# Kernel tuning notes

Hardware: AMD Instinct MI355X
Metric: run time of the kernel (lower is better)

Reference implementation:

```python
import jax, jax.numpy as jnp
import numpy as np

N_NODES = 50_000
N_EDGES = 1_600_000
N_VMS = 10_000
N_SCORE = 1_000_000
D_IN, D_E, D_OUT = 128, 64, 64
MLP_IN, MLP_H, MLP_OUT = 64, 128, 64
H1, H2 = 50, 25  # GNNTower fixed hidden widths


def setup_inputs() -> dict:
    key = jax.random.key(0)
    ks = jax.random.split(key, 24)
    w = lambda k, s: (jax.random.normal(k, s, jnp.float32) * 0.05)
    return {
        "component_features": jax.random.normal(ks[0], (N_NODES, D_IN), jnp.float32),
        "component_edges_features": jax.random.normal(ks[1], (N_EDGES, D_E), jnp.float32),
        "vm_features": jax.random.normal(ks[2], (N_VMS, MLP_IN), jnp.float32),
        "src": jax.random.randint(ks[3], (N_EDGES,), 0, N_NODES, jnp.int32),
        "dst": jax.random.randint(ks[4], (N_EDGES,), 0, N_NODES, jnp.int32),
        "e_comp": jax.random.randint(ks[5], (N_SCORE,), 0, N_NODES, jnp.int32),
        "e_vm": jax.random.randint(ks[6], (N_SCORE,), 0, N_VMS, jnp.int32),
        # GNN layer 1: W_msg [D_IN+D_E, H1], W_apply [D_IN+H1, H1]
        "Wm1": w(ks[7], (D_IN + D_E, H1)), "bm1": jnp.zeros((H1,), jnp.float32),
        "Wa1": w(ks[8], (D_IN + H1, H1)), "ba1": jnp.zeros((H1,), jnp.float32),
        # GNN layer 2
        "Wm2": w(ks[9], (H1 + D_E, H2)), "bm2": jnp.zeros((H2,), jnp.float32),
        "Wa2": w(ks[10], (H1 + H2, H2)), "ba2": jnp.zeros((H2,), jnp.float32),
        # GNN layer 3
        "Wm3": w(ks[11], (H2 + D_E, D_OUT)), "bm3": jnp.zeros((D_OUT,), jnp.float32),
        "Wa3": w(ks[12], (H2 + D_OUT, D_OUT)), "ba3": jnp.zeros((D_OUT,), jnp.float32),
        # MLP tower
        "Wmlp1": w(ks[13], (MLP_IN, MLP_H)), "bmlp1": jnp.zeros((MLP_H,), jnp.float32),
        "Wmlp2": w(ks[14], (MLP_H, MLP_OUT)), "bmlp2": jnp.zeros((MLP_OUT,), jnp.float32),
    }


def reference(component_features, component_edges_features, vm_features,
              src, dst, e_comp, e_vm,
              Wm1, bm1, Wa1, ba1, Wm2, bm2, Wa2, ba2, Wm3, bm3, Wa3, ba3,
              Wmlp1, bmlp1, Wmlp2, bmlp2):
    ef = component_edges_features

    def gnn_layer(h, Wm, bm, Wa, ba):
        d = h.shape[-1]
        # message: relu(W_msg @ concat(h[src], efeat)) == gather + split matmul (avoids concat copy)
        m = jax.nn.relu(h[src] @ Wm[:d] + ef @ Wm[d:] + bm)  # [E, out]
        # scatter-sum aggregation into destination nodes
        h_neigh = jax.ops.segment_sum(m, dst, num_segments=N_NODES)  # [N, out]
        # apply: relu(W_apply @ concat(h, h_neigh))
        return jax.nn.relu(h @ Wa[:d] + h_neigh @ Wa[d:] + ba)

    h = gnn_layer(component_features, Wm1, bm1, Wa1, ba1)   # [N, 50]
    h = gnn_layer(h, Wm2, bm2, Wa2, ba2)                    # [N, 25]  (dropout = identity in eval)
    h = gnn_layer(h, Wm3, bm3, Wa3, ba3)                    # [N, D_OUT]

    vm = jax.nn.relu(vm_features @ Wmlp1 + bmlp1) @ Wmlp2 + bmlp2  # [V, MLP_OUT]

    # sum over concat(comp_emb[e_comp], vm_emb[e_vm]) == sum of parts
    scores = jnp.sum(h, axis=-1)[e_comp] + jnp.sum(vm, axis=-1)[e_vm]  # [N_SCORE]
    return jax.nn.sigmoid(scores)
```

## Files before the change

### kernel.cpp

```cpp
#include <hip/hip_runtime.h>

typedef unsigned int uint;
typedef unsigned short ushort;
typedef short bf16x8 __attribute__((ext_vector_type(8)));
typedef float f32x4  __attribute__((ext_vector_type(4)));


__device__ __forceinline__ ushort f2bf(float f) {
    uint u = __float_as_uint(f);
    u += 0x7FFFu + ((u >> 16) & 1u);
    return (ushort)(u >> 16);
}
__device__ __forceinline__ float bf2f(uint s) {
    return __uint_as_float(s << 16);
}

template<int K0, int KP0, int K1, int KP1, int KC, int OUT, int WOUT,
         int NTC, int RPT, int MODE>
__global__ __launch_bounds__(256) void tile_gemm(
    const float* __restrict__ X0, int sx0,
    const float* __restrict__ X1, int sx1,
    const float* __restrict__ Wg, const float* __restrict__ Bg,
    float* __restrict__ Y, int sy, int nR)
{
    constexpr int KPT  = KP0 + KP1;
    constexpr int C4   = KC / 4;
    constexpr int OUTP = 4 * NTC;
    constexpr int NTR  = 256 / NTC;
    constexpr int TR   = NTR * RPT;
    static_assert(TR == 128, "tile must be 128 rows");
    static_assert(KPT % KC == 0, "KC must divide KPT");

    __shared__ float4 Xl[TR * C4];
    __shared__ float4 Wl[KC * NTC];
    __shared__ float  __align__(16) bl[OUTP];

    const int tid = threadIdx.x;
    const int r0  = blockIdx.x * TR;

    for (int idx = tid; idx < OUTP; idx += 256)
        bl[idx] = (Bg != nullptr && idx < OUT) ? Bg[idx] : 0.f;

    const int tc  = tid & (NTC - 1);
    const int tr  = tid / NTC;
    const int key = (RPT * tr) >> 3;

    float4 acc[RPT];
    #pragma unroll
    for (int i = 0; i < RPT; i++) acc[i] = make_float4(0.f, 0.f, 0.f, 0.f);

    for (int kc0 = 0; kc0 < KPT; kc0 += KC) {
        if (kc0 != 0) __syncthreads();
        for (int idx = tid; idx < TR * C4; idx += 256) {
            int r = idx / C4, c = idx - r * C4;
            int col = kc0 + 4 * c;
            int gr = r0 + r;
            float4 v = make_float4(0.f, 0.f, 0.f, 0.f);
            if (gr < nR) {
                if (KP1 == 0 || col < KP0)
                    v = *reinterpret_cast<const float4*>(X0 + (long long)gr * sx0 + col);
                else
                    v = *reinterpret_cast<const float4*>(X1 + (long long)gr * sx1 + (col - KP0));
            }
            int cs = c + ((r >> 3) % C4); if (cs >= C4) cs -= C4;
            Xl[r * C4 + cs] = v;
        }
        for (int idx = tid; idx < KC * OUTP; idx += 256) {
            int kl = idx / OUTP, o = idx - kl * OUTP;
            int k = kc0 + kl;
            float v = 0.f;
            if (o < OUT) {
                if (k < KP0) { if (k < K0) v = Wg[k * OUT + o]; }
                else { int kk = k - KP0; if (kk < K1) v = Wg[(K0 + kk) * OUT + o]; }
            }
            ((float*)Wl)[kl * OUTP + o] = v;
        }
        __syncthreads();

        const int km = key % C4;
        #pragma unroll 4
        for (int k4 = 0; k4 < C4; k4++) {
            int cs = k4 + km; if (cs >= C4) cs -= C4;
            float4 x[RPT];
            #pragma unroll
            for (int i = 0; i < RPT; i++)
                x[i] = Xl[(RPT * tr + i) * C4 + cs];
            #pragma unroll
            for (int kk = 0; kk < 4; kk++) {
                float4 w = Wl[(4 * k4 + kk) * NTC + tc];
                #pragma unroll
                for (int i = 0; i < RPT; i++) {
                    float xs = (kk == 0) ? x[i].x : (kk == 1) ? x[i].y
                             : (kk == 2) ? x[i].z : x[i].w;
                    acc[i].x = fmaf(xs, w.x, acc[i].x);
                    acc[i].y = fmaf(xs, w.y, acc[i].y);
                    acc[i].z = fmaf(xs, w.z, acc[i].z);
                    acc[i].w = fmaf(xs, w.w, acc[i].w);
                }
            }
        }
    }

    const float4 b4 = reinterpret_cast<float4*>(bl)[tc];
    const int o = 4 * tc;

    if (MODE == 0 || MODE == 1) {
        if (o < WOUT) {
            #pragma unroll
            for (int i = 0; i < RPT; i++) {
                int gr = r0 + RPT * tr + i;
                if (gr < nR) {
                    float4 v;
                    v.x = acc[i].x + b4.x; v.y = acc[i].y + b4.y;
                    v.z = acc[i].z + b4.z; v.w = acc[i].w + b4.w;
                    if (MODE == 1) {
                        v.x = fmaxf(v.x, 0.f); v.y = fmaxf(v.y, 0.f);
                        v.z = fmaxf(v.z, 0.f); v.w = fmaxf(v.w, 0.f);
                    }
                    *reinterpret_cast<float4*>(Y + (long long)gr * sy + o) = v;
                }
            }
        }
    } else {
        #pragma unroll
        for (int i = 0; i < RPT; i++) {
            int gr = r0 + RPT * tr + i;
            float s = fmaxf(acc[i].x + b4.x, 0.f) + fmaxf(acc[i].y + b4.y, 0.f)
                    + fmaxf(acc[i].z + b4.z, 0.f) + fmaxf(acc[i].w + b4.w, 0.f);
            #pragma unroll
            for (int off = 1; off < NTC; off <<= 1) s += __shfl_xor(s, off);
            if (tc == 0 && gr < nR) Y[gr] = s;
        }
    }
}

template<int NT, bool SECB>
__global__ __launch_bounds__(256) void proj_mfma(
    const float* __restrict__ ef,
    const float* __restrict__ WA, int wacols,
    const float* __restrict__ WB, int wbcols,
    const int* __restrict__ invperm,
    ushort* __restrict__ GA, ushort* __restrict__ GB, int nE)
{
    constexpr int NCOL = NT * 16;
    constexpr int CLP  = NCOL + 8;
    constexpr int CPR  = NCOL / 8;
    constexpr int GAS  = SECB ? 64 : NCOL;

    __shared__ ushort Al[64 * 64];
    __shared__ ushort Bl[NT * 128 * 8];
    __shared__ ushort Cl[64 * CLP];
    __shared__ int    sl_pos[64];

    const int tid = threadIdx.x;

    for (int idx = tid; idx < NT * 128; idx += 256) {
        int t  = idx >> 7;
        int ks = (idx >> 6) & 1;
        int l  = idx & 63;
        int col = t * 16 + (l & 15);
        int kb  = ks * 32 + ((l >> 4) << 3);
        ushort u[8];
        #pragma unroll
        for (int j = 0; j < 8; j++) {
            int k = kb + j;
            float w = 0.f;
            if (!SECB || col < 64) { if (col < wacols) w = WA[k * wacols + col]; }
            else { int c2 = col - 64; if (c2 < wbcols) w = WB[k * wbcols + c2]; }
            u[j] = f2bf(w);
        }
        *reinterpret_cast<bf16x8*>(&Bl[idx * 8]) = *reinterpret_cast<bf16x8*>(u);
    }

    const int wv = tid >> 6;
    const int l  = tid & 63;
    const int ntiles = (nE + 63) >> 6;

    for (int tile = blockIdx.x; tile < ntiles; tile += gridDim.x) {
        const int r0 = tile << 6;
        __syncthreads();

        if (tid < 64) sl_pos[tid] = (r0 + tid < nE) ? invperm[r0 + tid] : -1;
        {
            int row = tid >> 2;
            int kq  = (tid & 3) << 4;
            int gr  = r0 + row;
            float4 f0 = {0,0,0,0}, f1 = {0,0,0,0}, f2 = {0,0,0,0}, f3 = {0,0,0,0};
            if (gr < nE) {
                const float* p = ef + (size_t)gr * 64 + kq;
                f0 = *reinterpret_cast<const float4*>(p);
                f1 = *reinterpret_cast<const float4*>(p + 4);
                f2 = *reinterpret_cast<const float4*>(p + 8);
                f3 = *reinterpret_cast<const float4*>(p + 12);
            }
            ushort u[16];
            u[0]=f2bf(f0.x); u[1]=f2bf(f0.y); u[2]=f2bf(f0.z); u[3]=f2bf(f0.w);
            u[4]=f2bf(f1.x); u[5]=f2bf(f1.y); u[6]=f2bf(f1.z); u[7]=f2bf(f1.w);
            u[8]=f2bf(f2.x); u[9]=f2bf(f2.y); u[10]=f2bf(f2.z); u[11]=f2bf(f2.w);
            u[12]=f2bf(f3.x); u[13]=f2bf(f3.y); u[14]=f2bf(f3.z); u[15]=f2bf(f3.w);
            int kc0 = ((kq >> 3) + 0) ^ (row & 7);
            int kc1 = ((kq >> 3) + 1) ^ (row & 7);
            *reinterpret_cast<bf16x8*>(&Al[(row << 6) + kc0 * 8]) = *reinterpret_cast<bf16x8*>(u);
            *reinterpret_cast<bf16x8*>(&Al[(row << 6) + kc1 * 8]) = *reinterpret_cast<bf16x8*>(u + 8);
        }
        __syncthreads();

        f32x4 acc[NT];
        #pragma unroll
        for (int t = 0; t < NT; t++) acc[t] = (f32x4){0.f, 0.f, 0.f, 0.f};
        const int rl = wv * 16 + (l & 15);
        #pragma unroll
        for (int ks = 0; ks < 2; ks++) {
            int kch = (ks * 4 + (l >> 4)) ^ (rl & 7);
            bf16x8 a = *reinterpret_cast<const bf16x8*>(&Al[(rl << 6) + kch * 8]);
            #pragma unroll
            for (int t = 0; t < NT; t++) {
                bf16x8 b = *reinterpret_cast<const bf16x8*>(&Bl[((t * 2 + ks) * 64 + l) * 8]);
                acc[t] = __builtin_amdgcn_mfma_f32_16x16x32_bf16(a, b, acc[t], 0, 0, 0);
            }
        }
        #pragma unroll
        for (int t = 0; t < NT; t++)
            #pragma unroll
            for (int j = 0; j < 4; j++) {
                int rr = wv * 16 + ((l >> 4) << 2) + j;
                Cl[rr * CLP + t * 16 + (l & 15)] = f2bf(acc[t][j]);
            }
        __syncthreads();

        for (int idx = tid; idx < 64 * CPR; idx += 256) {
            int row = idx / CPR, c = idx - row * CPR;
            int pos = sl_pos[row];
            if (pos < 0) continue;
            uint4 v = *reinterpret_cast<const uint4*>(&Cl[row * CLP + c * 8]);
            if (!SECB || c < 8)
                *reinterpret_cast<uint4*>(GA + (size_t)pos * GAS + c * 8) = v;
            else
                *reinterpret_cast<uint4*>(GB + (size_t)pos * 32 + (c - 8) * 8) = v;
        }
    }
}

template<int NCL, int GS, int SP>
__global__ __launch_bounds__(256) void agg_csr(
    const ushort* __restrict__ G, const int* __restrict__ srcp,
    const int* __restrict__ rowp, const float* __restrict__ P,
    float* __restrict__ ng, int nN)
{
    const int o = threadIdx.x & (NCL - 1);
    const int g = threadIdx.x / NCL;
    const int n = blockIdx.x * (256 / NCL) + g;
    if (n >= nN) return;
    const int s0 = rowp[n], s1 = rowp[n + 1];

    float a0=0,a1=0,a2=0,a3=0,a4=0,a5=0,a6=0,a7=0;
    int pos = s0;
    for (; pos + 2 <= s1; pos += 2) {
        int sA = srcp[pos], sB = srcp[pos + 1];
        uint4 gA = *reinterpret_cast<const uint4*>(G + (size_t)pos * GS + o * 8);
        uint4 gB = *reinterpret_cast<const uint4*>(G + (size_t)(pos + 1) * GS + o * 8);
        const float* pA = P + (size_t)sA * SP + o * 8;
        const float* pB = P + (size_t)sB * SP + o * 8;
        float4 pa0 = *reinterpret_cast<const float4*>(pA);
        float4 pa1 = *reinterpret_cast<const float4*>(pA + 4);
        float4 pb0 = *reinterpret_cast<const float4*>(pB);
        float4 pb1 = *reinterpret_cast<const float4*>(pB + 4);
        a0 += fmaxf(pa0.x + bf2f(gA.x & 0xffffu), 0.f) + fmaxf(pb0.x + bf2f(gB.x & 0xffffu), 0.f);
        a1 += fmaxf(pa0.y + bf2f(gA.x >> 16), 0.f)     + fmaxf(pb0.y + bf2f(gB.x >> 16), 0.f);
        a2 += fmaxf(pa0.z + bf2f(gA.y & 0xffffu), 0.f) + fmaxf(pb0.z + bf2f(gB.y & 0xffffu), 0.f);
        a3 += fmaxf(pa0.w + bf2f(gA.y >> 16), 0.f)     + fmaxf(pb0.w + bf2f(gB.y >> 16), 0.f);
        a4 += fmaxf(pa1.x + bf2f(gA.z & 0xffffu), 0.f) + fmaxf(pb1.x + bf2f(gB.z & 0xffffu), 0.f);
        a5 += fmaxf(pa1.y + bf2f(gA.z >> 16), 0.f)     + fmaxf(pb1.y + bf2f(gB.z >> 16), 0.f);
        a6 += fmaxf(pa1.z + bf2f(gA.w & 0xffffu), 0.f) + fmaxf(pb1.z + bf2f(gB.w & 0xffffu), 0.f);
        a7 += fmaxf(pa1.w + bf2f(gA.w >> 16), 0.f)     + fmaxf(pb1.w + bf2f(gB.w >> 16), 0.f);
    }
    if (pos < s1) {
        int sA = srcp[pos];
        uint4 gA = *reinterpret_cast<const uint4*>(G + (size_t)pos * GS + o * 8);
        const float* pA = P + (size_t)sA * SP + o * 8;
        float4 pa0 = *reinterpret_cast<const float4*>(pA);
        float4 pa1 = *reinterpret_cast<const float4*>(pA + 4);
        a0 += fmaxf(pa0.x + bf2f(gA.x & 0xffffu), 0.f);
        a1 += fmaxf(pa0.y + bf2f(gA.x >> 16), 0.f);
        a2 += fmaxf(pa0.z + bf2f(gA.y & 0xffffu), 0.f);
        a3 += fmaxf(pa0.w + bf2f(gA.y >> 16), 0.f);
        a4 += fmaxf(pa1.x + bf2f(gA.z & 0xffffu), 0.f);
        a5 += fmaxf(pa1.y + bf2f(gA.z >> 16), 0.f);
        a6 += fmaxf(pa1.z + bf2f(gA.w & 0xffffu), 0.f);
        a7 += fmaxf(pa1.w + bf2f(gA.w >> 16), 0.f);
    }
    float4 w0 = {a0, a1, a2, a3}, w1 = {a4, a5, a6, a7};
    float* yp = ng + (size_t)n * 64 + o * 8;
    *reinterpret_cast<float4*>(yp)     = w0;
    *reinterpret_cast<float4*>(yp + 4) = w1;
}

__global__ __launch_bounds__(256) void hist_kernel(
    const int* __restrict__ dst, int* __restrict__ deg, int nE)
{
    for (int e = blockIdx.x * 256 + threadIdx.x; e < nE; e += gridDim.x * 256)
        atomicAdd(&deg[dst[e]], 1);
}

__global__ __launch_bounds__(1024) void scan_kernel(
    const int* __restrict__ deg, int* __restrict__ rowp, int nN)
{
    __shared__ int wsum[16];
    __shared__ int carry;
    const int tid = threadIdx.x;
    if (tid == 0) carry = 0;
    __syncthreads();
    for (int base = 0; base < nN; base += 1024) {
        int x = (base + tid < nN) ? deg[base + tid] : 0;
        int v = x;
        #pragma unroll
        for (int off = 1; off < 64; off <<= 1) {
            int t = __shfl_up(v, off);
            if ((tid & 63) >= off) v += t;
        }
        if ((tid & 63) == 63) wsum[tid >> 6] = v;
        __syncthreads();
        if (tid < 16) {
            int t = wsum[tid];
            #pragma unroll
            for (int off = 1; off < 16; off <<= 1) {
                int u = __shfl_up(t, off);
                if (tid >= off) t += u;
            }
            wsum[tid] = t;
        }
        __syncthreads();
        int woff = (tid >= 64) ? wsum[(tid >> 6) - 1] : 0;
        int incl = v + woff + carry;
        if (base + tid < nN) rowp[base + tid] = incl - x;
        __syncthreads();
        if (tid == 1023) carry = incl;
        __syncthreads();
    }
    if (tid == 0) rowp[nN] = carry;
}

__global__ __launch_bounds__(256) void scatter_kernel(
    const int* __restrict__ src, const int* __restrict__ dst,
    const int* __restrict__ rowp, int* __restrict__ cursor,
    int* __restrict__ srcp, int* __restrict__ invperm, int nE)
{
    for (int e = blockIdx.x * 256 + threadIdx.x; e < nE; e += gridDim.x * 256) {
        int d = dst[e];
        int pos = rowp[d] + atomicAdd(&cursor[d], 1);
        srcp[pos] = src[e];
        invperm[e] = pos;
    }
}

__global__ void w2sum_kernel(const float* __restrict__ W2, const float* __restrict__ b2,
                             float* __restrict__ w2s)
{
    int j = threadIdx.x;
    float s = 0.f;
    for (int o = 0; o < 64; o++) s += W2[j * 64 + o];
    w2s[j] = s;
    if (j == 0) {
        float bs = 0.f;
        for (int o = 0; o < 64; o++) bs += b2[o];
        w2s[128] = bs;
    }
}

__global__ __launch_bounds__(256) void vm_kernel(
    const float* __restrict__ vmf, const float* __restrict__ W1,
    const float* __restrict__ b1, const float* __restrict__ w2s,
    float* __restrict__ vm_sum, int nV)
{
    const int lane = threadIdx.x & 63;
    const int grp  = threadIdx.x >> 6;
    for (int v = blockIdx.x * 4 + grp; v < nV; v += gridDim.x * 4) {
        const float* vr = vmf + (long long)v * 64;
        float a0 = b1[lane], a1 = b1[lane + 64];
        #pragma unroll 4
        for (int k = 0; k < 64; k += 4) {
            float4 x = *reinterpret_cast<const float4*>(vr + k);
            a0 = fmaf(x.x, W1[(k + 0) * 128 + lane], a0);
            a0 = fmaf(x.y, W1[(k + 1) * 128 + lane], a0);
            a0 = fmaf(x.z, W1[(k + 2) * 128 + lane], a0);
            a0 = fmaf(x.w, W1[(k + 3) * 128 + lane], a0);
            a1 = fmaf(x.x, W1[(k + 0) * 128 + lane + 64], a1);
            a1 = fmaf(x.y, W1[(k + 1) * 128 + lane + 64], a1);
            a1 = fmaf(x.z, W1[(k + 2) * 128 + lane + 64], a1);
            a1 = fmaf(x.w, W1[(k + 3) * 128 + lane + 64], a1);
        }
        float part = fmaxf(a0, 0.f) * w2s[lane] + fmaxf(a1, 0.f) * w2s[lane + 64];
        #pragma unroll
        for (int off = 32; off > 0; off >>= 1) part += __shfl_down(part, off);
        if (lane == 0) vm_sum[v] = part + w2s[128];
    }
}

__global__ __launch_bounds__(256) void score_kernel(
    const int* __restrict__ ec, const int* __restrict__ ev,
    const float* __restrict__ ns, const float* __restrict__ vs,
    float* __restrict__ out, int n)
{
    int i = blockIdx.x * blockDim.x + threadIdx.x;
    if (i < n) {
        float x = ns[ec[i]] + vs[ev[i]];
        out[i] = 1.f / (1.f + expf(-x));
    }
}

extern "C" void kernel_launch(void* const* d_in, const int* in_sizes, int n_in,
                              void* d_out, int out_size, void* d_ws, size_t ws_size,
                              hipStream_t stream)
{
    const float* comp = (const float*)d_in[0];
    const float* ef   = (const float*)d_in[1];
    const float* vmf  = (const float*)d_in[2];
    const int*   src  = (const int*)d_in[3];
    const int*   dst  = (const int*)d_in[4];
    const int*   ecmp = (const int*)d_in[5];
    const int*   evm  = (const int*)d_in[6];
    const float* Wm1 = (const float*)d_in[7];  const float* bm1 = (const float*)d_in[8];
    const float* Wa1 = (const float*)d_in[9];  const float* ba1 = (const float*)d_in[10];
    const float* Wm2 = (const float*)d_in[11]; const float* bm2 = (const float*)d_in[12];
    const float* Wa2 = (const float*)d_in[13]; const float* ba2 = (const float*)d_in[14];
    const float* Wm3 = (const float*)d_in[15]; const float* bm3 = (const float*)d_in[16];
    const float* Wa3 = (const float*)d_in[17]; const float* ba3 = (const float*)d_in[18];
    const float* W1  = (const float*)d_in[19]; const float* b1  = (const float*)d_in[20];
    const float* W2  = (const float*)d_in[21]; const float* b2  = (const float*)d_in[22];

    const int nN = in_sizes[0] / 128;
    const int nE = in_sizes[3];
    const int nV = in_sizes[2] / 64;
    const int nS = in_sizes[5];

    float* ws = (float*)d_ws;
    float* bufA     = ws;
    float* bufB     = bufA + (size_t)nN * 64;
    float* ng       = bufB + (size_t)nN * 64;
    float* node_sum = ng + (size_t)nN * 64;
    float* vm_sum   = node_sum + nN;
    float* w2s      = vm_sum + nV;
    int*   iws      = (int*)(w2s + 132);
    int*   deg      = iws;
    int*   rowp     = deg + nN;
    int*   cursor   = rowp + nN + 1;
    int*   srcp     = cursor + nN;
    int*   invperm  = srcp + nE;
    size_t Goff = (((size_t)((char*)(invperm + nE) - (char*)d_ws)) + 255) & ~(size_t)255;
    ushort* G1 = (ushort*)((char*)d_ws + Goff);
    ushort* G2 = G1 + (size_t)nE * 64;
    const bool twopass = (Goff + (size_t)nE * 96 * 2) <= ws_size;
    if (!twopass) G2 = G1;

    float* h1 = bufA;
    float* h2 = bufB;
    float* P1 = bufB;
    float* P2 = bufB;
    float* P3 = bufA;

    const float* We1 = Wm1 + 128 * 50;
    const float* We2 = Wm2 + 50 * 25;
    const float* We3 = Wm3 + 25 * 64;

    const int ngrid  = (nN + 127) / 128;
    const int ptiles = (nE + 63) / 64;
    const int pgrid  = ptiles < 2048 ? ptiles : 2048;
    const int a8grid = (nN * 8 + 255) / 256;
    const int a4grid = (nN * 4 + 255) / 256;
    const int sgrid  = (nE + 255) / 256 < 4096 ? (nE + 255) / 256 : 4096;

    hipMemsetAsync(deg, 0, (size_t)nN * sizeof(int), stream);
    hist_kernel<<<sgrid, 256, 0, stream>>>(dst, deg, nE);
    scan_kernel<<<1, 1024, 0, stream>>>(deg, rowp, nN);
    hipMemsetAsync(cursor, 0, (size_t)nN * sizeof(int), stream);
    scatter_kernel<<<sgrid, 256, 0, stream>>>(src, dst, rowp, cursor, srcp, invperm, nE);

    if (twopass)
        proj_mfma<6, true><<<pgrid, 256, 0, stream>>>(ef, We1, 50, We2, 25, invperm, G1, G2, nE);
    else
        proj_mfma<4, false><<<pgrid, 256, 0, stream>>>(ef, We1, 50, nullptr, 0, invperm, G1, nullptr, nE);

    tile_gemm<128,128, 0,0, 64, 50, 64, 16, 8, 0><<<ngrid, 256, 0, stream>>>(
        comp, 128, nullptr, 0, Wm1, bm1, P1, 64, nN);
    agg_csr<8, 64, 64><<<a8grid, 256, 0, stream>>>(G1, srcp, rowp, P1, ng, nN);
    if (!twopass)
        proj_mfma<2, false><<<pgrid, 256, 0, stream>>>(ef, We2, 25, nullptr, 0, invperm, G2, nullptr, nE);
    tile_gemm<128,128, 50,52, 60, 50, 52, 16, 8, 1><<<ngrid, 256, 0, stream>>>(
        comp, 128, ng, 64, Wa1, ba1, h1, 52, nN);
    if (twopass)
        proj_mfma<4, false><<<pgrid, 256, 0, stream>>>(ef, We3, 64, nullptr, 0, invperm, G1, nullptr, nE);

    tile_gemm<50,52, 0,0, 52, 25, 32, 8, 4, 0><<<ngrid, 256, 0, stream>>>(
        h1, 52, nullptr, 0, Wm2, bm2, P2, 32, nN);
    agg_csr<4, 32, 32><<<a4grid, 256, 0, stream>>>(G2, srcp, rowp, P2, ng, nN);
    if (!twopass)
        proj_mfma<4, false><<<pgrid, 256, 0, stream>>>(ef, We3, 64, nullptr, 0, invperm, G1, nullptr, nE);
    tile_gemm<50,52, 25,28, 80, 25, 28, 8, 4, 1><<<ngrid, 256, 0, stream>>>(
        h1, 52, ng, 64, Wa2, ba2, h2, 28, nN);

    tile_gemm<25,28, 0,0, 28, 64, 64, 16, 8, 0><<<ngrid, 256, 0, stream>>>(
        h2, 28, nullptr, 0, Wm3, bm3, P3, 64, nN);
    agg_csr<8, 64, 64><<<a8grid, 256, 0, stream>>>(G1, srcp, rowp, P3, ng, nN);
    tile_gemm<25,28, 64,68, 48, 64, 64, 16, 8, 2><<<ngrid, 256, 0, stream>>>(
        h2, 28, ng, 64, Wa3, ba3, node_sum, 1, nN);

    w2sum_kernel<<<1, 128, 0, stream>>>(W2, b2, w2s);
    vm_kernel<<<(nV + 3) / 4, 256, 0, stream>>>(vmf, W1, b1, w2s, vm_sum, nV);
    score_kernel<<<(nS + 255) / 256, 256, 0, stream>>>(ecmp, evm, node_sum, vm_sum, (float*)d_out, nS);
}
```

Before: 915.0 us.

## Fuse all three edge projections into one pass and parallelize CSR scan

Adds a proj_all kernel that projects edge features through all three layers' edge weights in one MFMA pass, reading the 1.6M×64 edge features once and writing three permuted bf16 buffers. Before, the fallback path read them twice. It is used when workspace is large enough, at the cost of more workspace memory and more LDS per block. It also replaces the single-block serial prefix scan with a three-kernel parallel block scan. The two memsets are merged by placing cursor next to deg.

```diff
diff --git a/kernel.cpp b/kernel.cpp
--- a/kernel.cpp
+++ b/kernel.cpp
@@ -130,6 +130,113 @@
             #pragma unroll
             for (int off = 1; off < NTC; off <<= 1) s += __shfl_xor(s, off);
             if (tc == 0 && gr < nR) Y[gr] = s;
+        }
+    }
+}
+
+__global__ __launch_bounds__(256) void proj_all(
+    const float* __restrict__ ef,
+    const float* __restrict__ W1e, const float* __restrict__ W2e,
+    const float* __restrict__ W3e, const int* __restrict__ invperm,
+    ushort* __restrict__ G1, ushort* __restrict__ G2, ushort* __restrict__ G3,
+    int nE)
+{
+    constexpr int NT  = 10;
+    constexpr int CLP = 168;
+
+    __shared__ ushort Al[64 * 64];
+    __shared__ ushort Bl[NT * 128 * 8];
+    __shared__ ushort Cl[64 * CLP];
+    __shared__ int    sl_pos[64];
+
+    const int tid = threadIdx.x;
+
+    for (int idx = tid; idx < NT * 128; idx += 256) {
+        int t  = idx >> 7;
+        int ks = (idx >> 6) & 1;
+        int l  = idx & 63;
+        int gp  = t * 16 + (l & 15);
+        int kb  = ks * 32 + ((l >> 4) << 3);
+        ushort u[8];
+        #pragma unroll
+        for (int j = 0; j < 8; j++) {
+            int k = kb + j;
+            float w = 0.f;
+            if (gp < 64)      { if (gp < 50) w = W1e[k * 50 + gp]; }
+            else if (gp < 96) { int c = gp - 64; if (c < 25) w = W2e[k * 25 + c]; }
+            else              { int c = gp - 96; w = W3e[k * 64 + c]; }
+            u[j] = f2bf(w);
+        }
+        *reinterpret_cast<bf16x8*>(&Bl[idx * 8]) = *reinterpret_cast<bf16x8*>(u);
+    }
+
+    const int wv = tid >> 6;
+    const int l  = tid & 63;
+    const int ntiles = (nE + 63) >> 6;
+
+    for (int tile = blockIdx.x; tile < ntiles; tile += gridDim.x) {
+        const int r0 = tile << 6;
+        __syncthreads();
+
+        if (tid < 64) sl_pos[tid] = (r0 + tid < nE) ? invperm[r0 + tid] : -1;
+        {
+            int row = tid >> 2;
+            int kq  = (tid & 3) << 4;
+            int gr  = r0 + row;
+            float4 f0 = {0,0,0,0}, f1 = {0,0,0,0}, f2 = {0,0,0,0}, f3 = {0,0,0,0};
+            if (gr < nE) {
+                const float* p = ef + (size_t)gr * 64 + kq;
+                f0 = *reinterpret_cast<const float4*>(p);
+                f1 = *reinterpret_cast<const float4*>(p + 4);
+                f2 = *reinterpret_cast<const float4*>(p + 8);
+                f3 = *reinterpret_cast<const float4*>(p + 12);
+            }
+            ushort u[16];
+            u[0]=f2bf(f0.x); u[1]=f2bf(f0.y); u[2]=f2bf(f0.z); u[3]=f2bf(f0.w);
+            u[4]=f2bf(f1.x); u[5]=f2bf(f1.y); u[6]=f2bf(f1.z); u[7]=f2bf(f1.w);
+            u[8]=f2bf(f2.x); u[9]=f2bf(f2.y); u[10]=f2bf(f2.z); u[11]=f2bf(f2.w);
+            u[12]=f2bf(f3.x); u[13]=f2bf(f3.y); u[14]=f2bf(f3.z); u[15]=f2bf(f3.w);
+            int kc0 = ((kq >> 3) + 0) ^ (row & 7);
+            int kc1 = ((kq >> 3) + 1) ^ (row & 7);
+            *reinterpret_cast<bf16x8*>(&Al[(row << 6) + kc0 * 8]) = *reinterpret_cast<bf16x8*>(u);
+            *reinterpret_cast<bf16x8*>(&Al[(row << 6) + kc1 * 8]) = *reinterpret_cast<bf16x8*>(u + 8);
+        }
+        __syncthreads();
+
+        f32x4 acc[NT];
+        #pragma unroll
+        for (int t = 0; t < NT; t++) acc[t] = (f32x4){0.f, 0.f, 0.f, 0.f};
+        const int rl = wv * 16 + (l & 15);
+        #pragma unroll
+        for (int ks = 0; ks < 2; ks++) {
+            int kch = (ks * 4 + (l >> 4)) ^ (rl & 7);
+            bf16x8 a = *reinterpret_cast<const bf16x8*>(&Al[(rl << 6) + kch * 8]);
+            #pragma unroll
+            for (int t = 0; t < NT; t++) {
+                bf16x8 b = *reinterpret_cast<const bf16x8*>(&Bl[((t * 2 + ks) * 64 + l) * 8]);
+                acc[t] = __builtin_amdgcn_mfma_f32_16x16x32_bf16(a, b, acc[t], 0, 0, 0);
+            }
+        }
+        #pragma unroll
+        for (int t = 0; t < NT; t++)
+            #pragma unroll
+            for (int j = 0; j < 4; j++) {
+                int rr = wv * 16 + ((l >> 4) << 2) + j;
+                Cl[rr * CLP + t * 16 + (l & 15)] = f2bf(acc[t][j]);
+            }
+        __syncthreads();
+
+        for (int idx = tid; idx < 64 * 20; idx += 256) {
+            int row = idx / 20, c = idx - row * 20;
+            int pos = sl_pos[row];
+            if (pos < 0) continue;
+            uint4 v = *reinterpret_cast<const uint4*>(&Cl[row * CLP + c * 8]);
+            if (c < 8)
+                *reinterpret_cast<uint4*>(G1 + (size_t)pos * 64 + c * 8) = v;
+            else if (c < 12)
+                *reinterpret_cast<uint4*>(G2 + (size_t)pos * 32 + (c - 8) * 8) = v;
+            else
+                *reinterpret_cast<uint4*>(G3 + (size_t)pos * 64 + (c - 12) * 8) = v;
         }
     }
 }
@@ -302,42 +409,78 @@
         atomicAdd(&deg[dst[e]], 1);
 }
 
-__global__ __launch_bounds__(1024) void scan_kernel(
-    const int* __restrict__ deg, int* __restrict__ rowp, int nN)
-{
-    __shared__ int wsum[16];
-    __shared__ int carry;
-    const int tid = threadIdx.x;
-    if (tid == 0) carry = 0;
+__global__ __launch_bounds__(256) void scan_blksum(
+    const int* __restrict__ deg, int* __restrict__ bsum, int nN)
+{
+    const int t = threadIdx.x;
+    const int base = blockIdx.x * 1024;
+    int s = 0;
+    for (int i = t; i < 1024; i += 256) {
+        int id = base + i;
+        s += (id < nN) ? deg[id] : 0;
+    }
+    #pragma unroll
+    for (int off = 32; off > 0; off >>= 1) s += __shfl_down(s, off);
+    __shared__ int w[4];
+    if ((t & 63) == 0) w[t >> 6] = s;
     __syncthreads();
-    for (int base = 0; base < nN; base += 1024) {
-        int x = (base + tid < nN) ? deg[base + tid] : 0;
-        int v = x;
-        #pragma unroll
-        for (int off = 1; off < 64; off <<= 1) {
-            int t = __shfl_up(v, off);
-            if ((tid & 63) >= off) v += t;
-        }
-        if ((tid & 63) == 63) wsum[tid >> 6] = v;
-        __syncthreads();
-        if (tid < 16) {
-            int t = wsum[tid];
-            #pragma unroll
-            for (int off = 1; off < 16; off <<= 1) {
-                int u = __shfl_up(t, off);
-                if (tid >= off) t += u;
-            }
-            wsum[tid] = t;
-        }
-        __syncthreads();
-        int woff = (tid >= 64) ? wsum[(tid >> 6) - 1] : 0;
-        int incl = v + woff + carry;
-        if (base + tid < nN) rowp[base + tid] = incl - x;
-        __syncthreads();
-        if (tid == 1023) carry = incl;
-        __syncthreads();
-    }
-    if (tid == 0) rowp[nN] = carry;
+    if (t == 0) bsum[blockIdx.x] = w[0] + w[1] + w[2] + w[3];
+}
+
+__global__ __launch_bounds__(256) void scan_top(
+    int* __restrict__ bsum, int nB, int* __restrict__ rowp, int nN)
+{
+    const int t = threadIdx.x;
+    int v = (t < nB) ? bsum[t] : 0;
+    int x = v;
+    #pragma unroll
+    for (int off = 1; off < 64; off <<= 1) {
+        int u = __shfl_up(x, off);
+        if ((t & 63) >= off) x += u;
+    }
+    __shared__ int wsum[4];
+    if ((t & 63) == 63) wsum[t >> 6] = x;
+    __syncthreads();
+    int add = 0;
+    #pragma unroll
+    for (int i = 0; i < 4; i++) if (i < (t >> 6)) add += wsum[i];
+    x += add;
+    if (t < nB) bsum[t] = x - v;
+    if (t == nB - 1) rowp[nN] = x;
+}
+
+__global__ __launch_bounds__(256) void scan_final(
+    const int* __restrict__ deg, const int* __restrict__ bsum,
+    int* __restrict__ rowp, int nN)
+{
+    const int t = threadIdx.x;
+    const int idx0 = blockIdx.x * 1024 + t * 4;
+    int e[4];
+    #pragma unroll
+    for (int i = 0; i < 4; i++) {
+        int id = idx0 + i;
+        e[i] = (id < nN) ? deg[id] : 0;
+    }
+    int tl = e[0] + e[1] + e[2] + e[3];
+    int x = tl;
+    #pragma unroll
+    for (int off = 1; off < 64; off <<= 1) {
+        int u = __shfl_up(x, off);
+        if ((t & 63) >= off) x += u;
+    }
+    __shared__ int wsum[4];
+    if ((t & 63) == 63) wsum[t >> 6] = x;
+    __syncthreads();
+    int add = 0;
+    #pragma unroll
+    for (int i = 0; i < 4; i++) if (i < (t >> 6)) add += wsum[i];
+    int run = (x - tl) + add + bsum[blockIdx.x];
+    #pragma unroll
+    for (int i = 0; i < 4; i++) {
+        int id = idx0 + i;
+        if (id < nN) rowp[id] = run;
+        run += e[i];
+    }
 }
 
 __global__ __launch_bounds__(256) void scatter_kernel(
@@ -442,15 +585,19 @@
     float* w2s      = vm_sum + nV;
     int*   iws      = (int*)(w2s + 132);
     int*   deg      = iws;
-    int*   rowp     = deg + nN;
-    int*   cursor   = rowp + nN + 1;
-    int*   srcp     = cursor + nN;
+    int*   cursor   = deg + nN;
+    int*   rowp     = cursor + nN;
+    int*   srcp     = rowp + nN + 1;
     int*   invperm  = srcp + nE;
-    size_t Goff = (((size_t)((char*)(invperm + nE) - (char*)d_ws)) + 255) & ~(size_t)255;
+    int*   bsum     = invperm + nE;
+    size_t Goff = (((size_t)((char*)(bsum + 256) - (char*)d_ws)) + 255) & ~(size_t)255;
     ushort* G1 = (ushort*)((char*)d_ws + Goff);
-    ushort* G2 = G1 + (size_t)nE * 64;
-    const bool twopass = (Goff + (size_t)nE * 96 * 2) <= ws_size;
-    if (!twopass) G2 = G1;
+    const size_t need_single = (size_t)nE * (64 + 32 + 64) * 2;
+    const bool single  = (Goff + need_single) <= ws_size;
+    const bool twopass = !single && (Goff + (size_t)nE * 96 * 2) <= ws_size;
+    ushort* G2 = single ? (G1 + (size_t)nE * 64)
+               : twopass ? (G1 + (size_t)nE * 64) : G1;
+    ushort* G3 = single ? (G2 + (size_t)nE * 32) : G1;
 
     float* h1 = bufA;
     float* h2 = bufB;
@@ -468,39 +615,44 @@
     const int a8grid = (nN * 8 + 255) / 256;
     const int a4grid = (nN * 4 + 255) / 256;
     const int sgrid  = (nE + 255) / 256 < 4096 ? (nE + 255) / 256 : 4096;
-
-    hipMemsetAsync(deg, 0, (size_t)nN * sizeof(int), stream);
+    const int nB     = (nN + 1023) / 1024;
+
+    hipMemsetAsync(deg, 0, (size_t)(2 * nN) * sizeof(int), stream);
     hist_kernel<<<sgrid, 256, 0, stream>>>(dst, deg, nE);
-    scan_kernel<<<1, 1024, 0, stream>>>(deg, rowp, nN);
-    hipMemsetAsync(cursor, 0, (size_t)nN * sizeof(int), stream);
+    scan_blksum<<<nB, 256, 0, stream>>>(deg, bsum, nN);
+    scan_top<<<1, 256, 0, stream>>>(bsum, nB, rowp, nN);
+    scan_final<<<nB, 256, 0, stream>>>(deg, bsum, rowp, nN);
     scatter_kernel<<<sgrid, 256, 0, stream>>>(src, dst, rowp, cursor, srcp, invperm, nE);
 
-    if (twopass)
+    if (single) {
+        proj_all<<<pgrid, 256, 0, stream>>>(ef, We1, We2, We3, invperm, G1, G2, G3, nE);
+    } else if (twopass) {
         proj_mfma<6, true><<<pgrid, 256, 0, stream>>>(ef, We1, 50, We2, 25, invperm, G1, G2, nE);
-    else
+    } else {
         proj_mfma<4, false><<<pgrid, 256, 0, stream>>>(ef, We1, 50, nullptr, 0, invperm, G1, nullptr, nE);
+    }
 
     tile_gemm<128,128, 0,0, 64, 50, 64, 16, 8, 0><<<ngrid, 256, 0, stream>>>(
         comp, 128, nullptr, 0, Wm1, bm1, P1, 64, nN);
     agg_csr<8, 64, 64><<<a8grid, 256, 0, stream>>>(G1, srcp, rowp, P1, ng, nN);
-    if (!twopass)
+    if (!single && !twopass)
         proj_mfma<2, false><<<pgrid, 256, 0, stream>>>(ef, We2, 25, nullptr, 0, invperm, G2, nullptr, nE);
     tile_gemm<128,128, 50,52, 60, 50, 52, 16, 8, 1><<<ngrid, 256, 0, stream>>>(
         comp, 128, ng, 64, Wa1, ba1, h1, 52, nN);
-    if (twopass)
+    if (!single && twopass)
         proj_mfma<4, false><<<pgrid, 256, 0, stream>>>(ef, We3, 64, nullptr, 0, invperm, G1, nullptr, nE);
 
     tile_gemm<50,52, 0,0, 52, 25, 32, 8, 4, 0><<<ngrid, 256, 0, stream>>>(
         h1, 52, nullptr, 0, Wm2, bm2, P2, 32, nN);
     agg_csr<4, 32, 32><<<a4grid, 256, 0, stream>>>(G2, srcp, rowp, P2, ng, nN);
-    if (!twopass)
+    if (!single && !twopass)
         proj_mfma<4, false><<<pgrid, 256, 0, stream>>>(ef, We3, 64, nullptr, 0, invperm, G1, nullptr, nE);
     tile_gemm<50,52, 25,28, 80, 25, 28, 8, 4, 1><<<ngrid, 256, 0, stream>>>(
         h1, 52, ng, 64, Wa2, ba2, h2, 28, nN);
 
     tile_gemm<25,28, 0,0, 28, 64, 64, 16, 8, 0><<<ngrid, 256, 0, stream>>>(
         h2, 28, nullptr, 0, Wm3, bm3, P3, 64, nN);
-    agg_csr<8, 64, 64><<<a8grid, 256, 0, stream>>>(G1, srcp, rowp, P3, ng, nN);
+    agg_csr<8, 64, 64><<<a8grid, 256, 0, stream>>>(G3, srcp, rowp, P3, ng, nN);
     tile_gemm<25,28, 64,68, 48, 64, 64, 16, 8, 2><<<ngrid, 256, 0, stream>>>(
         h2, 28, ng, 64, Wa3, ba3, node_sum, 1, nN);
 
```

Result: faster. 802.6 us (-12.3%).
